# Performance work log

Hardware: AMD Instinct MI355X
Metric: run time of the kernel (lower is better)

The kernel has to match this reference:

```python
import jax, jax.numpy as jnp
import numpy as np

B, C, H, W = 4, 64, 128, 128
NP = 9        # num_param (N offset points per pixel)
OUTC = 128
STRIDE = 1
EPS = 1e-5    # BatchNorm eps


def _conv(x, w, b=None, stride=1):
    out = jax.lax.conv_general_dilated(
        x, w, (stride, stride), 'SAME',
        dimension_numbers=('NCHW', 'OIHW', 'NCHW'))
    if b is not None:
        out = out + b[None, :, None, None]
    return out


def setup_inputs() -> dict:
    key = jax.random.key(0)
    ks = jax.random.split(key, 6)
    s = lambda k, sh, sc: jax.random.normal(k, sh, jnp.float32) * sc
    return dict(
        x=s(ks[0], (B, C, H, W), 1.0),
        p_w=s(ks[1], (2 * NP, C, 3, 3), 0.02),   # offset conv (3x3, pad 1)
        p_b=s(ks[2], (2 * NP,), 0.02),
        conv_w=s(ks[3], (OUTC, C, 1, 1), 0.05),  # final 1x1 conv, no bias
        bn_gamma=jnp.ones((OUTC,), jnp.float32),
        bn_beta=jnp.zeros((OUTC,), jnp.float32),
        attn_w=s(ks[4], (1, C, 1, 1), 0.05),
        attn_b=s(ks[5], (1,), 0.05),
    )


def _forward(x, p_w, p_b, conv_w, bn_gamma, bn_beta, attn_w, attn_b):
    N = NP
    # density attention (computed as in source; adaptive re-parameterization skipped)
    density = jax.nn.sigmoid(_conv(x, attn_w, attn_b))  # noqa: F841

    # learned offsets: [B, 2N, H, W] (first N channels = row/x, last N = col/y)
    offset = _conv(x, p_w, p_b, stride=STRIDE)

    # p_n: base kernel grid offsets (row-major 3x3 -> values 0..2)
    base_int = int(round(np.sqrt(NP)))
    row_number = NP // base_int
    ii, jj = np.meshgrid(np.arange(row_number), np.arange(base_int), indexing='ij')
    p_n = jnp.asarray(np.concatenate([ii.ravel(), jj.ravel()]).astype(np.float32))  # [2N]

    # p_0: per-pixel base coordinates
    p0x = jnp.broadcast_to(jnp.arange(H, dtype=jnp.float32)[:, None] * STRIDE, (H, W))
    p0y = jnp.broadcast_to(jnp.arange(W, dtype=jnp.float32)[None, :] * STRIDE, (H, W))
    p_0 = jnp.concatenate([jnp.broadcast_to(p0x, (N, H, W)),
                           jnp.broadcast_to(p0y, (N, H, W))], axis=0)  # [2N,H,W]

    # sampling locations p: [B, H, W, 2N]
    p = (offset + p_n[None, :, None, None] + p_0[None]).transpose(0, 2, 3, 1)

    q_lt = jax.lax.stop_gradient(jnp.floor(p))   # detached, as in source
    q_rb = q_lt + 1.0
    px, py = p[..., :N], p[..., N:]
    ltx, lty = q_lt[..., :N], q_lt[..., N:]
    rbx, rby = q_rb[..., :N], q_rb[..., N:]

    # bilinear weights
    g_lt = (1 + (ltx - px)) * (1 + (lty - py))
    g_rb = (1 - (rbx - px)) * (1 - (rby - py))
    g_lb = (1 + (ltx - px)) * (1 - (rby - py))
    g_rt = (1 - (rbx - px)) * (1 + (lty - py))

    HW = H * W
    x_flat = x.reshape(B, C, HW)

    def gather(qx, qy):
        idx = jnp.clip((qx * W + qy).astype(jnp.int32), 0, HW - 1)  # [B,H,W,N]
        idx = idx.reshape(B, -1)
        out = jax.vmap(lambda xf, ix: xf[:, ix])(x_flat, idx)       # [B,C,H*W*N]
        return out.reshape(B, C, H, W, N)

    x_off = (g_lt[:, None] * gather(ltx, lty)
             + g_rb[:, None] * gather(rbx, rby)
             + g_lb[:, None] * gather(ltx, rby)
             + g_rt[:, None] * gather(rbx, lty))    # [B,C,H,W,N]

    # rearrange 'b c h w n -> b c (h n) w'
    x_off = x_off.transpose(0, 1, 2, 4, 3).reshape(B, C, H * N, W)

    # 1x1 conv (no bias) + BatchNorm2d (training-mode batch stats) + SiLU
    y = _conv(x_off, conv_w)
    mean = y.mean(axis=(0, 2, 3))
    var = y.var(axis=(0, 2, 3))  # biased, as torch BN uses for normalization
    y = (y - mean[None, :, None, None]) * jax.lax.rsqrt(var[None, :, None, None] + EPS)
    y = y * bn_gamma[None, :, None, None] + bn_beta[None, :, None, None]
    return jax.nn.silu(y)


def reference(x, p_w, p_b, conv_w, bn_gamma, bn_beta, attn_w, attn_b):
    return _forward(x, p_w, p_b, conv_w, bn_gamma, bn_beta, attn_w, attn_b)
```

## Files before the change

kernel.cpp:

```cpp
#include <hip/hip_runtime.h>

#define CIN   64
#define NOUT  128
#define IMH   128
#define IMW   128
#define NPTS  9
#define NB    4
#define HW    (IMH*IMW)
#define ROWS  (IMH*NPTS)
#define CHS   (ROWS*IMW)
#define TOTAL ((size_t)NB*NOUT*CHS)

typedef float f32x4 __attribute__((ext_vector_type(4)));

__global__ __launch_bounds__(256) void k_offset(const float* __restrict__ x,
                                                const float* __restrict__ pw,
                                                const float* __restrict__ pb,
                                                float* __restrict__ off) {
    __shared__ float wl[576 * 19];
    __shared__ float red[3 * 64 * 19];

    int tid = threadIdx.x;
    for (int t = tid; t < 18 * 576; t += 256) {
        int k = t / 576, cj = t % 576;
        wl[cj * 19 + k] = pw[t];
    }
    __syncthreads();

    int cg = tid >> 6;
    int lp = tid & 63;
    int gid = blockIdx.x * 64 + lp;
    int b = gid >> 14;
    int hw = gid & 16383;
    int h = hw >> 7;
    int w = hw & 127;

    float acc[18];
#pragma unroll
    for (int k = 0; k < 18; ++k) acc[k] = (cg == 0) ? pb[k] : 0.f;

    const float* xb = x + (size_t)b * CIN * HW;
    int c0 = cg * 16;
    for (int c = c0; c < c0 + 16; ++c) {
        const float* xc = xb + c * HW;
#pragma unroll
        for (int dh = 0; dh < 3; ++dh) {
            int hh = h + dh - 1;
            if ((unsigned)hh >= 128u) continue;
#pragma unroll
            for (int dw = 0; dw < 3; ++dw) {
                int ww = w + dw - 1;
                if ((unsigned)ww >= 128u) continue;
                float xv = xc[hh * IMW + ww];
                const float* wr = &wl[(c * 9 + dh * 3 + dw) * 19];
#pragma unroll
                for (int k = 0; k < 18; ++k) acc[k] += wr[k] * xv;
            }
        }
    }

    if (cg > 0) {
        float* rp = &red[((cg - 1) * 64 + lp) * 19];
#pragma unroll
        for (int k = 0; k < 18; ++k) rp[k] = acc[k];
    }
    __syncthreads();
    if (cg == 0) {
#pragma unroll
        for (int k = 0; k < 18; ++k)
            acc[k] += red[(0 * 64 + lp) * 19 + k] + red[(64 + lp) * 19 + k] + red[(128 + lp) * 19 + k];
        float* ob = off + (size_t)b * 18 * HW + hw;
#pragma unroll
        for (int k = 0; k < 18; ++k) ob[k * HW] = acc[k];
    }
}

__global__ __launch_bounds__(256) void k_z(const float* __restrict__ x,
                                           const float* __restrict__ cw,
                                           float* __restrict__ z) {
    __shared__ float xs[64 * 128];
    __shared__ float wsm[64 * 128];
    int tid = threadIdx.x;
    int b   = blockIdx.x >> 7;
    int hw0 = (blockIdx.x & 127) << 7;

    const float* xb = x + (size_t)b * CIN * HW + hw0;
#pragma unroll
    for (int i = 0; i < 32; ++i) {
        int t = tid + i * 256;
        int c = t >> 7, l = t & 127;
        xs[t] = xb[c * HW + l];
    }
#pragma unroll
    for (int i = 0; i < 32; ++i) {
        int t = tid + i * 256;
        int oc = t & 127, c = t >> 7;
        wsm[c * 128 + oc] = cw[oc * 64 + c];
    }
    __syncthreads();

    int hw4  = (tid & 31) << 2;
    int oc16 = (tid >> 5) << 4;

    float acc[4][16];
#pragma unroll
    for (int j = 0; j < 4; ++j)
#pragma unroll
        for (int k = 0; k < 16; ++k) acc[j][k] = 0.f;

    for (int c = 0; c < 64; ++c) {
        float4 xv = *(const float4*)&xs[c * 128 + hw4];
        float xq[4] = {xv.x, xv.y, xv.z, xv.w};
        float wv[16];
        const float4* wrow = (const float4*)&wsm[c * 128 + oc16];
#pragma unroll
        for (int m = 0; m < 4; ++m) ((float4*)wv)[m] = wrow[m];
#pragma unroll
        for (int j = 0; j < 4; ++j)
#pragma unroll
            for (int k = 0; k < 16; ++k) acc[j][k] += xq[j] * wv[k];
    }

#pragma unroll
    for (int j = 0; j < 4; ++j) {
        size_t rowb = ((size_t)b * HW + hw0 + hw4 + j) * NOUT + oc16;
        float4* zp = (float4*)&z[rowb];
#pragma unroll
        for (int m = 0; m < 4; ++m)
            zp[m] = make_float4(acc[j][4*m], acc[j][4*m+1], acc[j][4*m+2], acc[j][4*m+3]);
    }
}

__device__ __forceinline__ void bilin_setup(const float* __restrict__ off,
                                            int b, int h, int n, int w,
                                            float4& g, int4& id) {
    const float* ob = off + ((size_t)b * 18 + n) * HW + h * IMW + w;
    float ox = ob[0];
    float oy = ob[9 * HW];
    float px = ox + (float)(n / 3) + (float)h;
    float py = oy + (float)(n % 3) + (float)w;
    float fX = floorf(px), fY = floorf(py);
    float fx = px - fX, fy = py - fY;
    int X = (int)fX, Y = (int)fY;
    g.x = (1.f - fx) * (1.f - fy);
    g.y = fx * fy;
    g.z = (1.f - fx) * fy;
    g.w = fx * (1.f - fy);
    id.x = min(max(X * IMW + Y, 0), HW - 1) * NOUT;
    id.y = min(max((X + 1) * IMW + (Y + 1), 0), HW - 1) * NOUT;
    id.z = min(max(X * IMW + (Y + 1), 0), HW - 1) * NOUT;
    id.w = min(max((X + 1) * IMW + Y, 0), HW - 1) * NOUT;
}

__device__ __forceinline__ int swz_block() {
    return (blockIdx.x & 7) * 576 + (blockIdx.x >> 3);
}

__global__ __launch_bounds__(256) void k_sum(const float* __restrict__ off,
                                             const float* __restrict__ z,
                                             float* __restrict__ gsum,
                                             float* __restrict__ gsq) {
    int logical = swz_block();
    int n  = logical % 9;
    int t2 = logical / 9;
    int h  = t2 & 127;
    int b  = t2 >> 7;

    __shared__ float4 gS[128];
    __shared__ int4   iS[128];
    __shared__ float  lsum[128];
    __shared__ float  lsq[128];

    int tid = threadIdx.x;
    if (tid < 128) {
        lsum[tid] = 0.f; lsq[tid] = 0.f;
        float4 g; int4 id;
        bilin_setup(off, b, h, n, tid, g, id);
        gS[tid] = g; iS[tid] = id;
    }
    __syncthreads();

    int g32 = tid >> 5;
    int c4  = (tid & 31) << 2;
    const float* zb = z + (size_t)b * HW * NOUT + c4;

    float s0=0, s1=0, s2=0, s3=0, q0=0, q1=0, q2=0, q3=0;

    float4 plt, prb, plb, prt;
    {
        int4 id = iS[g32];
        plt = *(const float4*)(zb + id.x);
        prb = *(const float4*)(zb + id.y);
        plb = *(const float4*)(zb + id.z);
        prt = *(const float4*)(zb + id.w);
    }
#pragma unroll
    for (int wi = 0; wi < 16; ++wi) {
        float4 nlt, nrb, nlb, nrt;
        if (wi < 15) {
            int4 idn = iS[((wi + 1) << 3) + g32];
            nlt = *(const float4*)(zb + idn.x);
            nrb = *(const float4*)(zb + idn.y);
            nlb = *(const float4*)(zb + idn.z);
            nrt = *(const float4*)(zb + idn.w);
        }
        float4 g = gS[(wi << 3) + g32];
        float a0 = g.x*plt.x + g.y*prb.x + g.z*plb.x + g.w*prt.x;
        float a1 = g.x*plt.y + g.y*prb.y + g.z*plb.y + g.w*prt.y;
        float a2 = g.x*plt.z + g.y*prb.z + g.z*plb.z + g.w*prt.z;
        float a3 = g.x*plt.w + g.y*prb.w + g.z*plb.w + g.w*prt.w;
        s0 += a0; q0 += a0*a0;
        s1 += a1; q1 += a1*a1;
        s2 += a2; q2 += a2*a2;
        s3 += a3; q3 += a3*a3;
        plt = nlt; prb = nrb; plb = nlb; prt = nrt;
    }
    atomicAdd(&lsum[c4],     s0);
    atomicAdd(&lsum[c4 + 1], s1);
    atomicAdd(&lsum[c4 + 2], s2);
    atomicAdd(&lsum[c4 + 3], s3);
    atomicAdd(&lsq[c4],      q0);
    atomicAdd(&lsq[c4 + 1],  q1);
    atomicAdd(&lsq[c4 + 2],  q2);
    atomicAdd(&lsq[c4 + 3],  q3);
    __syncthreads();
    if (tid < 128)       atomicAdd(&gsum[tid],      lsum[tid]);
    else                 atomicAdd(&gsq[tid - 128], lsq[tid - 128]);
}

__global__ void k_stats(const float* __restrict__ gsum, const float* __restrict__ gsq,
                        const float* __restrict__ gamma, const float* __restrict__ beta,
                        float* __restrict__ scale, float* __restrict__ shift) {
    int c = threadIdx.x;
    const float cnt = (float)(NB * ROWS * IMW);
    float m = gsum[c] / cnt;
    float v = gsq[c] / cnt - m * m;
    float inv = rsqrtf(fmaxf(v, 0.f) + 1e-5f);
    float sc = inv * gamma[c];
    scale[c] = sc;
    shift[c] = beta[c] - m * sc;
}

__global__ __launch_bounds__(256) void k_apply(const float* __restrict__ off,
                                               const float* __restrict__ z,
                                               const float* __restrict__ scale,
                                               const float* __restrict__ shift,
                                               float* __restrict__ out) {
    int logical = swz_block();
    int n  = logical % 9;
    int t2 = logical / 9;
    int h  = t2 & 127;
    int b  = t2 >> 7;

    __shared__ float4 gS[128];
    __shared__ int4   iS[128];
    __shared__ float  ybuf[32 * 132];

    int tid = threadIdx.x;
    if (tid < 128) {
        float4 g; int4 id;
        bilin_setup(off, b, h, n, tid, g, id);
        gS[tid] = g; iS[tid] = id;
    }
    __syncthreads();

    int ws = tid >> 5;
    int c4 = (tid & 31) << 2;
    float4 sc = *(const float4*)&scale[c4];
    float4 sh = *(const float4*)&shift[c4];
    const float* zb = z + (size_t)b * HW * NOUT + c4;
    int r = h * 9 + n;
    float* outr = out + (size_t)b * NOUT * CHS + (size_t)r * IMW;

    for (int chunk = 0; chunk < 4; ++chunk) {
        int w0 = chunk << 5;
#pragma unroll
        for (int jj = 0; jj < 4; ++jj) {
            int wl  = (jj << 3) + ws;
            int w   = w0 + wl;
            float4 g = gS[w];
            int4  id = iS[w];
            float4 vlt = *(const float4*)(zb + id.x);
            float4 vrb = *(const float4*)(zb + id.y);
            float4 vlb = *(const float4*)(zb + id.z);
            float4 vrt = *(const float4*)(zb + id.w);
            float t0 = (g.x*vlt.x + g.y*vrb.x + g.z*vlb.x + g.w*vrt.x) * sc.x + sh.x;
            float t1 = (g.x*vlt.y + g.y*vrb.y + g.z*vlb.y + g.w*vrt.y) * sc.y + sh.y;
            float t2v= (g.x*vlt.z + g.y*vrb.z + g.z*vlb.z + g.w*vrt.z) * sc.z + sh.z;
            float t3 = (g.x*vlt.w + g.y*vrb.w + g.z*vlb.w + g.w*vrt.w) * sc.w + sh.w;
            float4 y;
            y.x = t0 / (1.f + __expf(-t0));
            y.y = t1 / (1.f + __expf(-t1));
            y.z = t2v / (1.f + __expf(-t2v));
            y.w = t3 / (1.f + __expf(-t3));
            *(float4*)&ybuf[wl * 132 + c4] = y;
        }
        __syncthreads();
#pragma unroll
        for (int i = 0; i < 4; ++i) {
            int task = (i << 8) + tid;
            int oc   = task >> 3;
            int w4   = (task & 7) << 2;
            f32x4 v;
            v.x = ybuf[(w4 + 0) * 132 + oc];
            v.y = ybuf[(w4 + 1) * 132 + oc];
            v.z = ybuf[(w4 + 2) * 132 + oc];
            v.w = ybuf[(w4 + 3) * 132 + oc];
            __builtin_nontemporal_store(v, (f32x4*)(outr + (size_t)oc * CHS + w0 + w4));
        }
        __syncthreads();
    }
}

extern "C" void kernel_launch(void* const* d_in, const int* in_sizes, int n_in,
                              void* d_out, int out_size, void* d_ws, size_t ws_size,
                              hipStream_t stream) {
    const float* x     = (const float*)d_in[0];
    const float* pw    = (const float*)d_in[1];
    const float* pb    = (const float*)d_in[2];
    const float* cw    = (const float*)d_in[3];
    const float* gamma = (const float*)d_in[4];
    const float* beta  = (const float*)d_in[5];

    float* out = (float*)d_out;
    float* ws  = (float*)d_ws;

    float* off   = ws;
    float* z     = off + (size_t)NB * 18 * HW;
    float* gsum  = z + (size_t)NB * HW * NOUT;
    float* gsq   = gsum + NOUT;
    float* scale = gsq + NOUT;
    float* shift = scale + NOUT;

    hipLaunchKernelGGL(k_offset, dim3(1024), dim3(256), 0, stream, x, pw, pb, off);
    hipLaunchKernelGGL(k_z,      dim3(512),  dim3(256), 0, stream, x, cw, z);
    (void)hipMemsetAsync(gsum, 0, 2 * NOUT * sizeof(float), stream);
    hipLaunchKernelGGL(k_sum,    dim3(4608), dim3(256), 0, stream, off, z, gsum, gsq);
    hipLaunchKernelGGL(k_stats,  dim3(1),    dim3(128), 0, stream, gsum, gsq, gamma, beta, scale, shift);
    hipLaunchKernelGGL(k_apply,  dim3(4608), dim3(256), 0, stream, off, z, scale, shift, out);
}
```

Before: 328.8 us.

## Double-buffer apply kernel gathers, vectorize offset weight loads, fold memset into kernel

The apply kernel now double-buffers its shared transpose tile: it prefetches the four bilinear gathers for the next 32-column chunk into registers while the current chunk is written out, so each chunk needs one barrier instead of two. The offset-conv kernel pads its shared weight rows to 20 floats so each tap's 18 weights load as float4/float2 vectors. The separate memset of the BN accumulators is replaced by block 0 of the offset kernel zeroing them. In exchange the apply kernel uses more registers and twice the shared buffer, which may lower occupancy.

```diff
diff --git a/kernel.cpp b/kernel.cpp
--- a/kernel.cpp
+++ b/kernel.cpp
@@ -16,14 +16,17 @@
 __global__ __launch_bounds__(256) void k_offset(const float* __restrict__ x,
                                                 const float* __restrict__ pw,
                                                 const float* __restrict__ pb,
-                                                float* __restrict__ off) {
-    __shared__ float wl[576 * 19];
+                                                float* __restrict__ off,
+                                                float* __restrict__ stats0) {
+    __shared__ float wl[576 * 20];
     __shared__ float red[3 * 64 * 19];
 
     int tid = threadIdx.x;
+    if (blockIdx.x == 0) stats0[tid] = 0.f;
+
     for (int t = tid; t < 18 * 576; t += 256) {
         int k = t / 576, cj = t % 576;
-        wl[cj * 19 + k] = pw[t];
+        wl[cj * 20 + k] = pw[t];
     }
     __syncthreads();
 
@@ -52,9 +55,15 @@
                 int ww = w + dw - 1;
                 if ((unsigned)ww >= 128u) continue;
                 float xv = xc[hh * IMW + ww];
-                const float* wr = &wl[(c * 9 + dh * 3 + dw) * 19];
-#pragma unroll
-                for (int k = 0; k < 18; ++k) acc[k] += wr[k] * xv;
+                const float* wr = &wl[(c * 9 + dh * 3 + dw) * 20];
+                float wv[18];
+                *(float4*)&wv[0]  = *(const float4*)(wr);
+                *(float4*)&wv[4]  = *(const float4*)(wr + 4);
+                *(float4*)&wv[8]  = *(const float4*)(wr + 8);
+                *(float4*)&wv[12] = *(const float4*)(wr + 12);
+                *(float2*)&wv[16] = *(const float2*)(wr + 16);
+#pragma unroll
+                for (int k = 0; k < 18; ++k) acc[k] += wv[k] * xv;
             }
         }
     }
@@ -241,6 +250,27 @@
     shift[c] = beta[c] - m * sc;
 }
 
+__device__ __forceinline__ void proc_store(float4 vlt, float4 vrb, float4 vlb, float4 vrt,
+                                           float4 g, float4 sc, float4 sh,
+                                           float* __restrict__ dst) {
+    float t0 = (g.x*vlt.x + g.y*vrb.x + g.z*vlb.x + g.w*vrt.x) * sc.x + sh.x;
+    float t1 = (g.x*vlt.y + g.y*vrb.y + g.z*vlb.y + g.w*vrt.y) * sc.y + sh.y;
+    float t2 = (g.x*vlt.z + g.y*vrb.z + g.z*vlb.z + g.w*vrt.z) * sc.z + sh.z;
+    float t3 = (g.x*vlt.w + g.y*vrb.w + g.z*vlb.w + g.w*vrt.w) * sc.w + sh.w;
+    float4 y;
+    y.x = t0 / (1.f + __expf(-t0));
+    y.y = t1 / (1.f + __expf(-t1));
+    y.z = t2 / (1.f + __expf(-t2));
+    y.w = t3 / (1.f + __expf(-t3));
+    *(float4*)dst = y;
+}
+
+#define GLOAD(P, wabs) { int4 _id = iS[wabs]; \
+    P##lt = *(const float4*)(zb + _id.x); \
+    P##rb = *(const float4*)(zb + _id.y); \
+    P##lb = *(const float4*)(zb + _id.z); \
+    P##rt = *(const float4*)(zb + _id.w); }
+
 __global__ __launch_bounds__(256) void k_apply(const float* __restrict__ off,
                                                const float* __restrict__ z,
                                                const float* __restrict__ scale,
@@ -254,7 +284,7 @@
 
     __shared__ float4 gS[128];
     __shared__ int4   iS[128];
-    __shared__ float  ybuf[32 * 132];
+    __shared__ float  ybuf[2][32 * 133];
 
     int tid = threadIdx.x;
     if (tid < 128) {
@@ -272,41 +302,50 @@
     int r = h * 9 + n;
     float* outr = out + (size_t)b * NOUT * CHS + (size_t)r * IMW;
 
+    float4 A0lt, A0rb, A0lb, A0rt;
+    float4 A1lt, A1rb, A1lb, A1rt;
+    float4 A2lt, A2rb, A2lb, A2rt;
+    float4 A3lt, A3rb, A3lb, A3rt;
+
+    GLOAD(A0, ws);       GLOAD(A1, 8 + ws);
+    GLOAD(A2, 16 + ws);  GLOAD(A3, 24 + ws);
+    proc_store(A0lt,A0rb,A0lb,A0rt, gS[ws],      sc, sh, &ybuf[0][(ws)      * 133 + c4]);
+    proc_store(A1lt,A1rb,A1lb,A1rt, gS[8 + ws],  sc, sh, &ybuf[0][(8 + ws)  * 133 + c4]);
+    proc_store(A2lt,A2rb,A2lb,A2rt, gS[16 + ws], sc, sh, &ybuf[0][(16 + ws) * 133 + c4]);
+    proc_store(A3lt,A3rb,A3lb,A3rt, gS[24 + ws], sc, sh, &ybuf[0][(24 + ws) * 133 + c4]);
+    __syncthreads();
+
+#pragma unroll
     for (int chunk = 0; chunk < 4; ++chunk) {
+        const int cur = chunk & 1;
+        const int nxt = cur ^ 1;
         int w0 = chunk << 5;
-#pragma unroll
-        for (int jj = 0; jj < 4; ++jj) {
-            int wl  = (jj << 3) + ws;
-            int w   = w0 + wl;
-            float4 g = gS[w];
-            int4  id = iS[w];
-            float4 vlt = *(const float4*)(zb + id.x);
-            float4 vrb = *(const float4*)(zb + id.y);
-            float4 vlb = *(const float4*)(zb + id.z);
-            float4 vrt = *(const float4*)(zb + id.w);
-            float t0 = (g.x*vlt.x + g.y*vrb.x + g.z*vlb.x + g.w*vrt.x) * sc.x + sh.x;
-            float t1 = (g.x*vlt.y + g.y*vrb.y + g.z*vlb.y + g.w*vrt.y) * sc.y + sh.y;
-            float t2v= (g.x*vlt.z + g.y*vrb.z + g.z*vlb.z + g.w*vrt.z) * sc.z + sh.z;
-            float t3 = (g.x*vlt.w + g.y*vrb.w + g.z*vlb.w + g.w*vrt.w) * sc.w + sh.w;
-            float4 y;
-            y.x = t0 / (1.f + __expf(-t0));
-            y.y = t1 / (1.f + __expf(-t1));
-            y.z = t2v / (1.f + __expf(-t2v));
-            y.w = t3 / (1.f + __expf(-t3));
-            *(float4*)&ybuf[wl * 132 + c4] = y;
-        }
-        __syncthreads();
+
+        if (chunk < 3) {
+            int wn = w0 + 32;
+            GLOAD(A0, wn + ws);       GLOAD(A1, wn + 8 + ws);
+            GLOAD(A2, wn + 16 + ws);  GLOAD(A3, wn + 24 + ws);
+        }
+
 #pragma unroll
         for (int i = 0; i < 4; ++i) {
             int task = (i << 8) + tid;
             int oc   = task >> 3;
             int w4   = (task & 7) << 2;
             f32x4 v;
-            v.x = ybuf[(w4 + 0) * 132 + oc];
-            v.y = ybuf[(w4 + 1) * 132 + oc];
-            v.z = ybuf[(w4 + 2) * 132 + oc];
-            v.w = ybuf[(w4 + 3) * 132 + oc];
+            v.x = ybuf[cur][(w4 + 0) * 133 + oc];
+            v.y = ybuf[cur][(w4 + 1) * 133 + oc];
+            v.z = ybuf[cur][(w4 + 2) * 133 + oc];
+            v.w = ybuf[cur][(w4 + 3) * 133 + oc];
             __builtin_nontemporal_store(v, (f32x4*)(outr + (size_t)oc * CHS + w0 + w4));
+        }
+
+        if (chunk < 3) {
+            int wn = w0 + 32;
+            proc_store(A0lt,A0rb,A0lb,A0rt, gS[wn + ws],      sc, sh, &ybuf[nxt][(ws)      * 133 + c4]);
+            proc_store(A1lt,A1rb,A1lb,A1rt, gS[wn + 8 + ws],  sc, sh, &ybuf[nxt][(8 + ws)  * 133 + c4]);
+            proc_store(A2lt,A2rb,A2lb,A2rt, gS[wn + 16 + ws], sc, sh, &ybuf[nxt][(16 + ws) * 133 + c4]);
+            proc_store(A3lt,A3rb,A3lb,A3rt, gS[wn + 24 + ws], sc, sh, &ybuf[nxt][(24 + ws) * 133 + c4]);
         }
         __syncthreads();
     }
@@ -332,9 +371,8 @@
     float* scale = gsq + NOUT;
     float* shift = scale + NOUT;
 
-    hipLaunchKernelGGL(k_offset, dim3(1024), dim3(256), 0, stream, x, pw, pb, off);
+    hipLaunchKernelGGL(k_offset, dim3(1024), dim3(256), 0, stream, x, pw, pb, off, gsum);
     hipLaunchKernelGGL(k_z,      dim3(512),  dim3(256), 0, stream, x, cw, z);
-    (void)hipMemsetAsync(gsum, 0, 2 * NOUT * sizeof(float), stream);
     hipLaunchKernelGGL(k_sum,    dim3(4608), dim3(256), 0, stream, off, z, gsum, gsq);
     hipLaunchKernelGGL(k_stats,  dim3(1),    dim3(128), 0, stream, gsum, gsq, gamma, beta, scale, shift);
     hipLaunchKernelGGL(k_apply,  dim3(4608), dim3(256), 0, stream, off, z, scale, shift, out);
```

Result: faster. 322.2 us (-2.0%).
